# Kernel tuning notes

Measured on AMD Instinct MI355X. Metric: run time of the kernel, lower is better.

The kernel has to match this reference:

```python
import jax, jax.numpy as jnp
import numpy as np

INPUT_SIZE = 1024
HIDDEN_SIZE = 1024
BATCH = 4096


def setup_inputs() -> dict:
    key = jax.random.key(0)
    ks = jax.random.split(key, 20)
    k = 1.0 / HIDDEN_SIZE
    bound = float(np.sqrt(k))

    def u(kk, shape):
        return jax.random.uniform(kk, shape, jnp.float32, -bound, bound)

    inp = {
        "x": jax.random.normal(ks[0], (BATCH, INPUT_SIZE), jnp.float32),
        "h0": jax.random.normal(ks[1], (BATCH, HIDDEN_SIZE), jnp.float32),
        "c0": jax.random.normal(ks[2], (BATCH, HIDDEN_SIZE), jnp.float32),
        "W_ii": u(ks[3], (INPUT_SIZE, HIDDEN_SIZE)), "b_ii": u(ks[4], (HIDDEN_SIZE,)),
        "W_if": u(ks[5], (INPUT_SIZE, HIDDEN_SIZE)), "b_if": u(ks[6], (HIDDEN_SIZE,)),
        "W_ig": u(ks[7], (INPUT_SIZE, HIDDEN_SIZE)), "b_ig": u(ks[8], (HIDDEN_SIZE,)),
        "W_io": u(ks[9], (INPUT_SIZE, HIDDEN_SIZE)), "b_io": u(ks[10], (HIDDEN_SIZE,)),
        "W_hi": u(ks[11], (HIDDEN_SIZE, HIDDEN_SIZE)), "b_hi": u(ks[12], (HIDDEN_SIZE,)),
        "W_hf": u(ks[13], (HIDDEN_SIZE, HIDDEN_SIZE)), "b_hf": u(ks[14], (HIDDEN_SIZE,)),
        "W_hg": u(ks[15], (HIDDEN_SIZE, HIDDEN_SIZE)), "b_hg": u(ks[16], (HIDDEN_SIZE,)),
        "W_ho": u(ks[17], (HIDDEN_SIZE, HIDDEN_SIZE)), "b_ho": u(ks[18], (HIDDEN_SIZE,)),
    }
    return inp


def reference(x, h0, c0,
              W_ii, b_ii, W_if, b_if, W_ig, b_ig, W_io, b_io,
              W_hi, b_hi, W_hf, b_hf, W_hg, b_hg, W_ho, b_ho):
    # Fuse the 4 input-side and 4 hidden-side GEMMs into two wide GEMMs,
    # then a single fused gate computation — same math as the original.
    Wi = jnp.concatenate([W_ii, W_if, W_ig, W_io], axis=1)  # [In, 4H]
    Wh = jnp.concatenate([W_hi, W_hf, W_hg, W_ho], axis=1)  # [H, 4H]
    b = jnp.concatenate([b_ii + b_hi, b_if + b_hf, b_ig + b_hg, b_io + b_ho])
    gates = x @ Wi + h0 @ Wh + b  # [B, 4H]
    zi, zf, zg, zo = jnp.split(gates, 4, axis=1)
    i = jax.nn.sigmoid(zi)
    f = jax.nn.sigmoid(zf)
    g = jnp.tanh(zg)
    o = jax.nn.sigmoid(zo)
    c1 = f * c0 + i * g
    h1 = o * c1
    return h1, c1
```

## Files before the change

kernel.cpp:

```cpp
#include <hip/hip_runtime.h>

typedef unsigned short u16;
typedef unsigned int u32;
typedef __attribute__((ext_vector_type(8))) short short8;
typedef __attribute__((ext_vector_type(4))) float f32x4;

__device__ __forceinline__ u16 f2b(float f) {
  u32 u = __builtin_bit_cast(u32, f);
  u32 r = (u + 0x7FFFu + ((u >> 16) & 1u)) >> 16;
  return (u16)r;
}

__device__ __forceinline__ void gl_lds16(const void* g, void* l) {
  __builtin_amdgcn_global_load_lds(
      (const __attribute__((address_space(1))) u32*)g,
      (__attribute__((address_space(3))) u32*)l, 16, 0, 0);
}

struct Ptrs8 { const float* p[8]; };

__global__ __launch_bounds__(256) void wt_pack(Ptrs8 w, u16* __restrict__ Wt) {
  __shared__ float lds[64 * 64];
  const int tid = threadIdx.x;
  const int bid = blockIdx.x;
  const int mat = bid >> 8;
  const int g = mat & 3, h = mat >> 2;
  const int tile = bid & 255;
  const int kt = tile >> 4, nt = tile & 15;
  const float* __restrict__ src = w.p[mat];

#pragma unroll
  for (int i = 0; i < 4; ++i) {
    int c = tid + i * 256;
    int k = c >> 4, n4 = (c & 15) * 4;
    gl_lds16(src + (size_t)(kt * 64 + k) * 1024 + nt * 64 + n4, &lds[c * 4]);
  }
  asm volatile("s_waitcnt vmcnt(0)");
  __syncthreads();

#pragma unroll
  for (int i = 0; i < 2; ++i) {
    int c = tid + i * 256;
    int n = c & 63, kb = (c >> 6) * 8;
    short8 v;
#pragma unroll
    for (int j = 0; j < 8; ++j) v[j] = (short)f2b(lds[(kb + j) * 64 + n]);
    size_t off = (size_t)(g * 1024 + nt * 64 + n) * 2048 + h * 1024 + kt * 64 + kb;
    *reinterpret_cast<short8*>(Wt + off) = v;
  }
}

__global__ __launch_bounds__(256) void xh_pack(const float* __restrict__ x,
                                               const float* __restrict__ h0,
                                               u16* __restrict__ Ap) {
  int t = blockIdx.x * 256 + threadIdx.x;
  int m = t >> 8, kc = t & 255;
  const float* src = (kc < 128) ? (x + (size_t)m * 1024 + kc * 8)
                                : (h0 + (size_t)m * 1024 + (kc - 128) * 8);
  float4 a = *reinterpret_cast<const float4*>(src);
  float4 b = *reinterpret_cast<const float4*>(src + 4);
  short8 v;
  v[0] = (short)f2b(a.x); v[1] = (short)f2b(a.y);
  v[2] = (short)f2b(a.z); v[3] = (short)f2b(a.w);
  v[4] = (short)f2b(b.x); v[5] = (short)f2b(b.y);
  v[6] = (short)f2b(b.z); v[7] = (short)f2b(b.w);
  *reinterpret_cast<short8*>(Ap + (size_t)m * 2048 + kc * 8) = v;
}

__global__ void bias_pack(Ptrs8 b, float* __restrict__ bias) {
  int i = blockIdx.x * 1024 + threadIdx.x;
  int g = i >> 10, n = i & 1023;
  bias[i] = b.p[g][n] + b.p[4 + g][n];
}

#define LD8(base, off) (*reinterpret_cast<const short8*>((base) + (off)))

__global__ __launch_bounds__(512, 2) void lstm_fused(
    const u16* __restrict__ Ap, const float* __restrict__ c0,
    const u16* __restrict__ Wt, const float* __restrict__ bias,
    float* __restrict__ out) {
  __shared__ u16 As[2][256 * 64];
  __shared__ u16 Bs[2][256 * 64];

  const int tid = threadIdx.x;
  const int lane = tid & 63;
  const int wid = tid >> 6;
  const int wr = wid >> 2;
  const int wc = wid & 3;
  const int fl = lane & 15;
  const int hi = lane >> 4;
  const int lo7 = fl & 7;

  const int bid0 = blockIdx.x;
  const int sbid = (bid0 & 7) * 32 + (bid0 >> 3);
  const int m0 = (sbid >> 4) * 256;
  const int n0 = (sbid & 15) * 64;

  int aoff[4], boff[4];
#pragma unroll
  for (int i = 0; i < 4; ++i) {
    const int L = tid + i * 512;
    const int r = L >> 3, cL = L & 7;
    const int cg = cL ^ (r & 7);
    aoff[i] = (m0 + r) * 2048 + cg * 8;
    const int wce = r >> 6, ge = (r >> 4) & 3, ue = r & 15;
    boff[i] = (ge * 1024 + n0 + wce * 16 + ue) * 2048 + cg * 8;
  }

  auto stageA = [&](int buf, int t) {
    const int k0 = t * 64;
#pragma unroll
    for (int i = 0; i < 4; ++i)
      gl_lds16(Ap + aoff[i] + k0, &As[buf][(tid + i * 512) * 8]);
  };
  auto stageB = [&](int buf, int t) {
    const int k0 = t * 64;
#pragma unroll
    for (int i = 0; i < 4; ++i)
      gl_lds16(Wt + boff[i] + k0, &Bs[buf][(tid + i * 512) * 8]);
  };

  const int c0k = (hi ^ lo7) * 8;
  const int c1k = ((4 + hi) ^ lo7) * 8;
  const int arow = (wr * 128 + fl) * 64;
  const int brow = (wc * 64 + fl) * 64;

  f32x4 acc[8][4] = {};

  stageA(0, 0);
  stageB(0, 0);
  stageA(1, 1);
  stageB(1, 1);

  for (int t = 0; t < 32; ++t) {
    const int cur = t & 1;
    const u16* Ab = &As[cur][0];
    const u16* Bb = &Bs[cur][0];

    if (t < 31) {
      asm volatile("s_waitcnt vmcnt(8)" ::: "memory");
    } else {
      asm volatile("s_waitcnt vmcnt(0)" ::: "memory");
    }
    __builtin_amdgcn_s_barrier();

    short8 bf[4][2];
#pragma unroll
    for (int g = 0; g < 4; ++g) {
      bf[g][0] = LD8(Bb, brow + g * 1024 + c0k);
      bf[g][1] = LD8(Bb, brow + g * 1024 + c1k);
    }
    short8 af[8][2];
#pragma unroll
    for (int mi = 0; mi < 8; ++mi) {
      af[mi][0] = LD8(Ab, arow + mi * 1024 + c0k);
      af[mi][1] = LD8(Ab, arow + mi * 1024 + c1k);
    }
    asm volatile("s_waitcnt lgkmcnt(0)" ::: "memory");
    __builtin_amdgcn_s_barrier();

    if (t < 30) {
      stageA(cur, t + 2);
      stageB(cur, t + 2);
    }

    __builtin_amdgcn_s_setprio(1);
#pragma unroll
    for (int mi = 0; mi < 8; ++mi)
#pragma unroll
      for (int g = 0; g < 4; ++g) {
        acc[mi][g] = __builtin_amdgcn_mfma_f32_16x16x32_bf16(
            af[mi][0], bf[g][0], acc[mi][g], 0, 0, 0);
        acc[mi][g] = __builtin_amdgcn_mfma_f32_16x16x32_bf16(
            af[mi][1], bf[g][1], acc[mi][g], 0, 0, 0);
      }
    __builtin_amdgcn_s_setprio(0);
  }

  const int col = n0 + wc * 16 + fl;
  float bv[4];
#pragma unroll
  for (int g = 0; g < 4; ++g) bv[g] = bias[g * 1024 + col];

#pragma unroll
  for (int mi = 0; mi < 8; ++mi) {
#pragma unroll
    for (int r = 0; r < 4; ++r) {
      const int row = m0 + wr * 128 + mi * 16 + hi * 4 + r;
      const float zi = acc[mi][0][r] + bv[0];
      const float zf = acc[mi][1][r] + bv[1];
      const float zg = acc[mi][2][r] + bv[2];
      const float zo = acc[mi][3][r] + bv[3];
      const float ig = 1.f / (1.f + __expf(-zi));
      const float fg = 1.f / (1.f + __expf(-zf));
      const float gg = 1.f - 2.f / (__expf(2.f * zg) + 1.f);
      const float og = 1.f / (1.f + __expf(-zo));
      const float c0v = c0[(size_t)row * 1024 + col];
      const float c1 = fg * c0v + ig * gg;
      const float h1 = og * c1;
      out[(size_t)row * 1024 + col] = h1;
      out[(size_t)4194304 + (size_t)row * 1024 + col] = c1;
    }
  }
}

extern "C" void kernel_launch(void* const* d_in, const int* in_sizes, int n_in,
                              void* d_out, int out_size, void* d_ws, size_t ws_size,
                              hipStream_t stream) {
  const float* x  = (const float*)d_in[0];
  const float* h0 = (const float*)d_in[1];
  const float* c0 = (const float*)d_in[2];
  Ptrs8 w, b;
  for (int i = 0; i < 4; ++i) {
    w.p[i]     = (const float*)d_in[3 + 2 * i];
    b.p[i]     = (const float*)d_in[4 + 2 * i];
    w.p[4 + i] = (const float*)d_in[11 + 2 * i];
    b.p[4 + i] = (const float*)d_in[12 + 2 * i];
  }
  u16* Wt = (u16*)d_ws;
  u16* Ap = (u16*)((char*)d_ws + (size_t)4096 * 2048 * 2);
  float* bias = (float*)((char*)d_ws + (size_t)2 * 4096 * 2048 * 2);
  float* out = (float*)d_out;

  wt_pack<<<2048, 256, 0, stream>>>(w, Wt);
  xh_pack<<<4096, 256, 0, stream>>>(x, h0, Ap);
  bias_pack<<<4, 1024, 0, stream>>>(b, bias);
  lstm_fused<<<256, 512, 0, stream>>>(Ap, c0, Wt, bias, out);
}
```

Before: 93.63 us.

## Split GEMM k-step into four quadrant phases with interleaved staging

Restructures the main loop into four sub-phases per k-tile. Each phase reads only the A or B fragments it needs from LDS, issues part of the next tile's global-to-LDS loads, and runs a quarter of the MFMAs, in the style of an 8-wave ping-pong schedule. The B tile layout in LDS is reordered so gate groups are contiguous. The aim is to overlap LDS reads and global loads with MFMA work and to cut register pressure from holding all fragments at once. The cost is extra barriers per tile, and the vmcnt accounting is fragile.

```diff
diff --git a/kernel.cpp b/kernel.cpp
--- a/kernel.cpp
+++ b/kernel.cpp
@@ -74,6 +74,30 @@
 }
 
 #define LD8(base, off) (*reinterpret_cast<const short8*>((base) + (off)))
+#define MFMA_(a, b, c) __builtin_amdgcn_mfma_f32_16x16x32_bf16(a, b, c, 0, 0, 0)
+
+#define READ_A(DST, BASE)                                   \
+  _Pragma("unroll")                                         \
+  for (int mi = 0; mi < 4; ++mi) {                          \
+    DST[mi][0] = LD8(Ab, arow + (BASE + mi) * 1024 + c0k);  \
+    DST[mi][1] = LD8(Ab, arow + (BASE + mi) * 1024 + c1k);  \
+  }
+#define READ_B(DST, GB)                                     \
+  _Pragma("unroll")                                         \
+  for (int g = 0; g < 2; ++g) {                             \
+    DST[g][0] = LD8(Bb, bbase + (GB + g) * 4096 + c0k);     \
+    DST[g][1] = LD8(Bb, bbase + (GB + g) * 4096 + c1k);     \
+  }
+#define MFMA_QUAD(AF, BF, MO, GO)                                              \
+  __builtin_amdgcn_s_setprio(1);                                               \
+  _Pragma("unroll")                                                            \
+  for (int mi = 0; mi < 4; ++mi)                                               \
+    _Pragma("unroll")                                                          \
+    for (int g = 0; g < 2; ++g) {                                              \
+      acc[MO + mi][GO + g] = MFMA_(AF[mi][0], BF[g][0], acc[MO + mi][GO + g]); \
+      acc[MO + mi][GO + g] = MFMA_(AF[mi][1], BF[g][1], acc[MO + mi][GO + g]); \
+    }                                                                          \
+  __builtin_amdgcn_s_setprio(0);
 
 __global__ __launch_bounds__(512, 2) void lstm_fused(
     const u16* __restrict__ Ap, const float* __restrict__ c0,
@@ -103,78 +127,86 @@
     const int r = L >> 3, cL = L & 7;
     const int cg = cL ^ (r & 7);
     aoff[i] = (m0 + r) * 2048 + cg * 8;
-    const int wce = r >> 6, ge = (r >> 4) & 3, ue = r & 15;
+    const int ge = r >> 6, wce = (r >> 4) & 3, ue = r & 15;
     boff[i] = (ge * 1024 + n0 + wce * 16 + ue) * 2048 + cg * 8;
   }
 
-  auto stageA = [&](int buf, int t) {
+  auto stageA = [&](int buf, int t, int h) {
     const int k0 = t * 64;
-#pragma unroll
-    for (int i = 0; i < 4; ++i)
-      gl_lds16(Ap + aoff[i] + k0, &As[buf][(tid + i * 512) * 8]);
+    gl_lds16(Ap + aoff[h] + k0, &As[buf][(tid + h * 512) * 8]);
+    gl_lds16(Ap + aoff[h + 2] + k0, &As[buf][(tid + (h + 2) * 512) * 8]);
   };
-  auto stageB = [&](int buf, int t) {
+  auto stageB = [&](int buf, int t, int h) {
     const int k0 = t * 64;
-#pragma unroll
-    for (int i = 0; i < 4; ++i)
-      gl_lds16(Wt + boff[i] + k0, &Bs[buf][(tid + i * 512) * 8]);
+    gl_lds16(Wt + boff[2 * h] + k0, &Bs[buf][(tid + (2 * h) * 512) * 8]);
+    gl_lds16(Wt + boff[2 * h + 1] + k0, &Bs[buf][(tid + (2 * h + 1) * 512) * 8]);
   };
 
   const int c0k = (hi ^ lo7) * 8;
   const int c1k = ((4 + hi) ^ lo7) * 8;
   const int arow = (wr * 128 + fl) * 64;
-  const int brow = (wc * 64 + fl) * 64;
+  const int bbase = (wc * 16 + fl) * 64;
 
   f32x4 acc[8][4] = {};
 
-  stageA(0, 0);
-  stageB(0, 0);
-  stageA(1, 1);
-  stageB(1, 1);
-
-  for (int t = 0; t < 32; ++t) {
-    const int cur = t & 1;
+  stageB(0, 0, 0);
+  stageA(0, 0, 0);
+  stageA(0, 0, 1);
+  stageB(0, 0, 1);
+
+  for (int t = 0; t < 31; ++t) {
+    const int cur = t & 1, nxt = cur ^ 1;
     const u16* Ab = &As[cur][0];
     const u16* Bb = &Bs[cur][0];
-
-    if (t < 31) {
-      asm volatile("s_waitcnt vmcnt(8)" ::: "memory");
-    } else {
-      asm volatile("s_waitcnt vmcnt(0)" ::: "memory");
-    }
-    __builtin_amdgcn_s_barrier();
-
-    short8 bf[4][2];
-#pragma unroll
-    for (int g = 0; g < 4; ++g) {
-      bf[g][0] = LD8(Bb, brow + g * 1024 + c0k);
-      bf[g][1] = LD8(Bb, brow + g * 1024 + c1k);
-    }
-    short8 af[8][2];
-#pragma unroll
-    for (int mi = 0; mi < 8; ++mi) {
-      af[mi][0] = LD8(Ab, arow + mi * 1024 + c0k);
-      af[mi][1] = LD8(Ab, arow + mi * 1024 + c1k);
-    }
-    asm volatile("s_waitcnt lgkmcnt(0)" ::: "memory");
-    __builtin_amdgcn_s_barrier();
-
-    if (t < 30) {
-      stageA(cur, t + 2);
-      stageB(cur, t + 2);
-    }
-
-    __builtin_amdgcn_s_setprio(1);
-#pragma unroll
-    for (int mi = 0; mi < 8; ++mi)
-#pragma unroll
-      for (int g = 0; g < 4; ++g) {
-        acc[mi][g] = __builtin_amdgcn_mfma_f32_16x16x32_bf16(
-            af[mi][0], bf[g][0], acc[mi][g], 0, 0, 0);
-        acc[mi][g] = __builtin_amdgcn_mfma_f32_16x16x32_bf16(
-            af[mi][1], bf[g][1], acc[mi][g], 0, 0, 0);
-      }
-    __builtin_amdgcn_s_setprio(0);
+    short8 af03[4][2], af47[4][2], bf01[2][2], bf23[2][2];
+
+    asm volatile("s_waitcnt vmcnt(4)" ::: "memory");
+    __builtin_amdgcn_s_barrier();
+    READ_A(af03, 0)
+    READ_B(bf01, 0)
+    stageB(nxt, t + 1, 0);
+    MFMA_QUAD(af03, bf01, 0, 0)
+
+    asm volatile("s_waitcnt vmcnt(4)" ::: "memory");
+    __builtin_amdgcn_s_barrier();
+    READ_A(af47, 4)
+    stageA(nxt, t + 1, 0);
+    MFMA_QUAD(af47, bf01, 4, 0)
+
+    asm volatile("s_waitcnt vmcnt(4)" ::: "memory");
+    __builtin_amdgcn_s_barrier();
+    READ_B(bf23, 2)
+    stageA(nxt, t + 1, 1);
+    MFMA_QUAD(af03, bf23, 0, 2)
+
+    __builtin_amdgcn_s_barrier();
+    stageB(nxt, t + 1, 1);
+    MFMA_QUAD(af47, bf23, 4, 2)
+  }
+
+  {
+    const u16* Ab = &As[1][0];
+    const u16* Bb = &Bs[1][0];
+    short8 af03[4][2], af47[4][2], bf01[2][2], bf23[2][2];
+
+    asm volatile("s_waitcnt vmcnt(4)" ::: "memory");
+    __builtin_amdgcn_s_barrier();
+    READ_A(af03, 0)
+    READ_B(bf01, 0)
+    MFMA_QUAD(af03, bf01, 0, 0)
+
+    asm volatile("s_waitcnt vmcnt(2)" ::: "memory");
+    __builtin_amdgcn_s_barrier();
+    READ_A(af47, 4)
+    MFMA_QUAD(af47, bf01, 4, 0)
+
+    asm volatile("s_waitcnt vmcnt(0)" ::: "memory");
+    __builtin_amdgcn_s_barrier();
+    READ_B(bf23, 2)
+    MFMA_QUAD(af03, bf23, 0, 2)
+
+    __builtin_amdgcn_s_barrier();
+    MFMA_QUAD(af47, bf23, 4, 2)
   }
 
   const int col = n0 + wc * 16 + fl;
```

Result: no change. 91.95 us (-1.8%).
